# Performance work log

Measured on AMD Instinct MI355X. Metric: run time of the kernel, lower is better.

## Reference

```python
import jax, jax.numpy as jnp
import numpy as np

N_HEADS = 16
D_MODEL = 1024
D_KV = 64


def setup_inputs() -> dict:
    key = jax.random.key(0)
    ks = jax.random.split(key, 5)
    x = jax.random.normal(ks[0], (4, 2048, D_MODEL), dtype=jnp.float32)
    # per-head projections stacked: [H, D_MODEL, D_KV]
    WQ = jax.random.normal(ks[1], (N_HEADS, D_MODEL, D_KV), dtype=jnp.float32) * (D_MODEL ** -0.5)
    WK = jax.random.normal(ks[2], (N_HEADS, D_MODEL, D_KV), dtype=jnp.float32) * (D_MODEL ** -0.5)
    WV = jax.random.normal(ks[3], (N_HEADS, D_MODEL, D_KV), dtype=jnp.float32) * (D_MODEL ** -0.5)
    WO = jax.random.normal(ks[4], (N_HEADS * D_KV, D_MODEL), dtype=jnp.float32) * ((N_HEADS * D_KV) ** -0.5)
    return {"x": x, "WQ": WQ, "WK": WK, "WV": WV, "WO": WO}


def reference(x, WQ, WK, WV, WO):
    # Batched over heads instead of the original per-head Python loop.
    # q,k,v: [B, H, S, Dk]
    q = jnp.einsum('bsd,hdk->bhsk', x, WQ)
    k = jnp.einsum('bsd,hdk->bhsk', x, WK)
    v = jnp.einsum('bsd,hdk->bhsk', x, WV)
    scale = 1.0 / jnp.sqrt(jnp.asarray(q.shape[-1], q.dtype))
    scores = jnp.einsum('bhqk,bhsk->bhqs', q, k) * scale  # [B, H, S, S]
    attn = jax.nn.softmax(scores, axis=-1)
    o = jnp.einsum('bhqs,bhsk->bhqk', attn, v)            # [B, H, S, Dk]
    # concat heads along feature dim == transpose + reshape
    B, H, S, Dk = o.shape
    o = o.transpose(0, 2, 1, 3).reshape(B, S, H * Dk)
    return o @ WO
```

## Files before the change

### kernel.cpp

```cpp
#include <hip/hip_runtime.h>
#include <stdint.h>
#include <stddef.h>


typedef __attribute__((ext_vector_type(8))) short short8;
typedef __attribute__((ext_vector_type(4))) float floatx4;
typedef __attribute__((ext_vector_type(16))) float floatx16;

#define MFMA_BF16(a, b, c) __builtin_amdgcn_mfma_f32_16x16x32_bf16((a), (b), (c), 0, 0, 0)
#define MFMA32_BF16(a, b, c) __builtin_amdgcn_mfma_f32_32x32x16_bf16((a), (b), (c), 0, 0, 0)

__device__ __forceinline__ unsigned short f32_bf16(float f) {
  union { float f; unsigned u; } v; v.f = f;
  unsigned r = v.u + 0x7fffu + ((v.u >> 16) & 1u);
  return (unsigned short)(r >> 16);
}

__device__ __forceinline__ unsigned pack_bf16_rh(float a, float b) {
  unsigned ua = __float_as_uint(a) + 0x8000u;
  unsigned ub = __float_as_uint(b) + 0x8000u;
  return __builtin_amdgcn_perm(ub, ua, 0x07060302u);
}

__device__ __forceinline__ float fast_exp2(float x) {
#if __has_builtin(__builtin_amdgcn_exp2f)
  return __builtin_amdgcn_exp2f(x);
#else
  return exp2f(x);
#endif
}

__device__ __forceinline__ void g2l16(const void* g, void* l) {
  __builtin_amdgcn_global_load_lds((const __attribute__((address_space(1))) void*)g,
                                   (__attribute__((address_space(3))) void*)l,
                                   16, 0, 0);
}


__global__ __launch_bounds__(256) void cvt_x_k(const float* __restrict__ x,
                                               unsigned short* __restrict__ xb) {
  int i = (blockIdx.x * 256 + threadIdx.x) * 4;
  float4 v = *(const float4*)(x + i);
  ushort4 o;
  o.x = f32_bf16(v.x); o.y = f32_bf16(v.y); o.z = f32_bf16(v.z); o.w = f32_bf16(v.w);
  *(ushort4*)(xb + i) = o;
}

__global__ __launch_bounds__(256) void cvt_w_k(const float* __restrict__ WQ,
                                               const float* __restrict__ WK,
                                               const float* __restrict__ WV,
                                               const float* __restrict__ WO,
                                               unsigned short* __restrict__ Wqkv,
                                               unsigned short* __restrict__ WOt) {
  __shared__ unsigned short tile[64][72];
  const int bid = blockIdx.x;
  const int tid = threadIdx.x;
  if (bid < 768) {
    const int th = bid >> 4;
    const int typ = th >> 4, h = th & 15;
    const float* W = (typ == 0) ? WQ : ((typ == 1) ? WK : WV);
    const float* src = W + ((size_t)h * 1024 + (bid & 15) * 64) * 64;
    #pragma unroll
    for (int it = 0; it < 16; ++it) {
      int f = it * 256 + tid;
      int dk = f & 63, dl = f >> 6;
      tile[dk][dl] = f32_bf16(src[(size_t)dl * 64 + dk]);
    }
    __syncthreads();
    unsigned short* dst = Wqkv + (size_t)(typ * 1024 + h * 64) * 1024 + (bid & 15) * 64;
    #pragma unroll
    for (int it = 0; it < 16; ++it) {
      int f = it * 256 + tid;
      int d = f & 63, dk = f >> 6;
      dst[(size_t)dk * 1024 + d] = tile[dk][d];
    }
  } else {
    const int id2 = bid - 768;
    const int nt = (id2 & 15) * 64, kt = (id2 >> 4) * 64;
    #pragma unroll
    for (int it = 0; it < 16; ++it) {
      int f = it * 256 + tid;
      int n = f & 63, kl = f >> 6;
      tile[n][kl] = f32_bf16(WO[(size_t)(kt + kl) * 1024 + nt + n]);
    }
    __syncthreads();
    #pragma unroll
    for (int it = 0; it < 16; ++it) {
      int f = it * 256 + tid;
      int k = f & 63, nl = f >> 6;
      WOt[(size_t)(nt + nl) * 1024 + kt + k] = tile[nl][k];
    }
  }
}


__global__ __launch_bounds__(256, 2)
void gemm_qkv_k(const unsigned short* __restrict__ A,
                const unsigned short* __restrict__ Bt,
                unsigned short* __restrict__ Qo,
                unsigned short* __restrict__ Ko,
                unsigned short* __restrict__ Vo) {
  __shared__ __align__(16) unsigned short As[8192];
  __shared__ __align__(16) unsigned short Bs[8192];
  const int lane = threadIdx.x & 63;
  const int wave = threadIdx.x >> 6;
  const int quad = lane >> 4;
  const int t = lane & 15;
  const int wm = wave >> 1, wn = wave & 1;
  const int row0 = blockIdx.y * 128;
  const int col0 = blockIdx.x * 128;

  floatx4 acc[4][4];
  #pragma unroll
  for (int i = 0; i < 4; ++i)
    #pragma unroll
    for (int j = 0; j < 4; ++j) acc[i][j] = (floatx4)0.0f;

  for (int k0 = 0; k0 < 1024; k0 += 64) {
    #pragma unroll
    for (int i = 0; i < 4; ++i) {
      int s = (wave * 4 + i) * 64 + lane;
      int r = s >> 3, kc = (s & 7) ^ (r & 7);
      g2l16(A  + (size_t)(row0 + r) * 1024 + k0 + kc * 8, As + (wave * 4 + i) * 512);
      g2l16(Bt + (size_t)(col0 + r) * 1024 + k0 + kc * 8, Bs + (wave * 4 + i) * 512);
    }
    __syncthreads();
    #pragma unroll
    for (int kk = 0; kk < 2; ++kk) {
      short8 af[4], bf[4];
      #pragma unroll
      for (int mt = 0; mt < 4; ++mt) {
        int r = wm * 64 + mt * 16 + t;
        int kc = (kk * 4 + quad) ^ (r & 7);
        af[mt] = *(const short8*)(As + (r * 8 + kc) * 8);
      }
      #pragma unroll
      for (int nt = 0; nt < 4; ++nt) {
        int r = wn * 64 + nt * 16 + t;
        int kc = (kk * 4 + quad) ^ (r & 7);
        bf[nt] = *(const short8*)(Bs + (r * 8 + kc) * 8);
      }
      #pragma unroll
      for (int mt = 0; mt < 4; ++mt)
        #pragma unroll
        for (int nt = 0; nt < 4; ++nt)
          acc[mt][nt] = MFMA_BF16(af[mt], bf[nt], acc[mt][nt]);
    }
    __syncthreads();
  }

  const int typ = col0 >> 10;
  const float qscale = 0.18033688011112042f;
  const int qp = ((quad & 1) << 1) | (quad >> 1);
  #pragma unroll
  for (int mt = 0; mt < 4; ++mt) {
    int grow0 = row0 + wm * 64 + mt * 16 + quad * 4;
    int b = grow0 >> 11;
    int s = grow0 & 2047;
    #pragma unroll
    for (int nt = 0; nt < 4; ++nt) {
      int gcol = col0 + wn * 64 + nt * 16 + t;
      int rem = gcol & 1023;
      int h = rem >> 6, dk = rem & 63;
      int bhh = b * 16 + h;
      if (typ == 0) {
        #pragma unroll
        for (int rg = 0; rg < 4; ++rg)
          Qo[((size_t)bhh * 2048 + s + rg) * 64 + dk] = f32_bf16(acc[mt][nt][rg] * qscale);
      } else if (typ == 1) {
        #pragma unroll
        for (int rg = 0; rg < 4; ++rg)
          Ko[((size_t)bhh * 2048 + s + rg) * 64 + dk] = f32_bf16(acc[mt][nt][rg]);
      } else {
        ushort4 pv;
        pv.x = f32_bf16(acc[mt][nt][0]);
        pv.y = f32_bf16(acc[mt][nt][1]);
        pv.z = f32_bf16(acc[mt][nt][2]);
        pv.w = f32_bf16(acc[mt][nt][3]);
        int sp = (s & ~15) | (qp << 2);
        *(ushort4*)(Vo + ((size_t)bhh * 64 + dk) * 2048 + sp) = pv;
      }
    }
  }
}


__global__ __launch_bounds__(256, 2)
void attn_k(const unsigned short* __restrict__ Qg_,
            const unsigned short* __restrict__ Kg_,
            const unsigned short* __restrict__ Vg_,
            unsigned short* __restrict__ O) {
  __shared__ __align__(16) char smem[32768];
  const int lane = threadIdx.x & 63;
  const int wave = threadIdx.x >> 6;
  const int h32 = lane >> 5;
  const int c32 = lane & 31;
  const int bh = blockIdx.x;
  const int q0 = blockIdx.y * 256;
  const unsigned short* Qg = Qg_ + ((size_t)bh * 2048 + q0) * 64;
  const unsigned short* Kg = Kg_ + (size_t)bh * 2048 * 64;
  const unsigned short* Vg = Vg_ + (size_t)bh * 64 * 2048;

  short8 qf[2][4];
  #pragma unroll
  for (int g = 0; g < 2; ++g) {
    int rq = wave * 64 + g * 32 + c32;
    #pragma unroll
    for (int dc = 0; dc < 4; ++dc)
      qf[g][dc] = *(const short8*)(Qg + (size_t)rq * 64 + dc * 16 + h32 * 8);
  }

  union { unsigned u[4]; short8 s8; } onesf;
  #pragma unroll
  for (int i = 0; i < 4; ++i) onesf.u[i] = 0x3F803F80u;

  floatx16 acc[2][2], accs[2];
  #pragma unroll
  for (int g = 0; g < 2; ++g) {
    acc[g][0] = (floatx16)0.0f; acc[g][1] = (floatx16)0.0f; accs[g] = (floatx16)0.0f;
  }

  for (int s0 = 0; s0 < 2048; s0 += 128) {
    #pragma unroll
    for (int i = 0; i < 4; ++i) {
      int s = (wave * 4 + i) * 64 + lane;
      int rk = s >> 3, ck = (s & 7) ^ (rk & 7);
      g2l16(Kg + (size_t)(s0 + rk) * 64 + ck * 8, smem + s * 16);
      int rv = s >> 4, cv = (s & 15) ^ (rv & 7);
      g2l16(Vg + (size_t)rv * 2048 + s0 + cv * 8, smem + 16384 + s * 16);
    }
    __syncthreads();

    #pragma unroll
    for (int kb = 0; kb < 4; ++kb) {
      floatx16 sc0 = (floatx16)0.0f, sc1 = (floatx16)0.0f;
      #pragma unroll
      for (int dc = 0; dc < 4; ++dc) {
        int rk = kb * 32 + c32;
        int kc = (dc * 2 + h32) ^ (rk & 7);
        short8 kf = *(const short8*)(smem + (rk * 8 + kc) * 16);
        sc0 = MFMA32_BF16(kf, qf[0][dc], sc0);
        sc1 = MFMA32_BF16(kf, qf[1][dc], sc1);
      }
      unsigned pk0[8], pk1[8];
      #pragma unroll
      for (int i = 0; i < 8; ++i) {
        float a0 = fast_exp2(sc0[2 * i]), b0 = fast_exp2(sc0[2 * i + 1]);
        float a1 = fast_exp2(sc1[2 * i]), b1 = fast_exp2(sc1[2 * i + 1]);
        pk0[i] = pack_bf16_rh(a0, b0);
        pk1[i] = pack_bf16_rh(a1, b1);
      }
      #pragma unroll
      for (int st = 0; st < 2; ++st) {
        union { unsigned u[4]; short8 s8; } af0, af1;
        #pragma unroll
        for (int i = 0; i < 4; ++i) { af0.u[i] = pk0[4 * st + i]; af1.u[i] = pk1[4 * st + i]; }
        int cc = kb * 4 + st * 2 + h32;
        #pragma unroll
        for (int nb = 0; nb < 2; ++nb) {
          int rv = nb * 32 + c32;
          short8 bv = *(const short8*)(smem + 16384 + (rv * 16 + (cc ^ (rv & 7))) * 16);
          acc[0][nb] = MFMA32_BF16(af0.s8, bv, acc[0][nb]);
          acc[1][nb] = MFMA32_BF16(af1.s8, bv, acc[1][nb]);
        }
        accs[0] = MFMA32_BF16(af0.s8, onesf.s8, accs[0]);
        accs[1] = MFMA32_BF16(af1.s8, onesf.s8, accs[1]);
      }
    }
    __syncthreads();
  }

  const int b = bh >> 4, h = bh & 15;
  #pragma unroll
  for (int g = 0; g < 2; ++g) {
    #pragma unroll
    for (int gg = 0; gg < 4; ++gg) {
      #pragma unroll
      for (int rr = 0; rr < 4; ++rr) {
        int qrel = rr + 8 * gg + 4 * h32;
        float rl = 1.0f / accs[g][4 * gg + rr];
        int token = b * 2048 + q0 + wave * 64 + g * 32 + qrel;
        size_t base = (size_t)token * 1024 + h * 64;
        O[base + c32]      = f32_bf16(acc[g][0][4 * gg + rr] * rl);
        O[base + 32 + c32] = f32_bf16(acc[g][1][4 * gg + rr] * rl);
      }
    }
  }
}


__global__ __launch_bounds__(256, 2)
void gemm_out_k(const unsigned short* __restrict__ A,
                const unsigned short* __restrict__ Bt,
                float* __restrict__ C) {
  __shared__ __align__(16) unsigned short As[8192];
  __shared__ __align__(16) unsigned short Bs[8192];
  const int lane = threadIdx.x & 63;
  const int wave = threadIdx.x >> 6;
  const int quad = lane >> 4;
  const int t = lane & 15;
  const int wm = wave >> 1, wn = wave & 1;
  const int row0 = blockIdx.y * 128;
  const int col0 = blockIdx.x * 128;

  floatx4 acc[4][4];
  #pragma unroll
  for (int i = 0; i < 4; ++i)
    #pragma unroll
    for (int j = 0; j < 4; ++j) acc[i][j] = (floatx4)0.0f;

  for (int k0 = 0; k0 < 1024; k0 += 64) {
    #pragma unroll
    for (int i = 0; i < 4; ++i) {
      int s = (wave * 4 + i) * 64 + lane;
      int r = s >> 3, kc = (s & 7) ^ (r & 7);
      g2l16(A  + (size_t)(row0 + r) * 1024 + k0 + kc * 8, As + (wave * 4 + i) * 512);
      g2l16(Bt + (size_t)(col0 + r) * 1024 + k0 + kc * 8, Bs + (wave * 4 + i) * 512);
    }
    __syncthreads();
    #pragma unroll
    for (int kk = 0; kk < 2; ++kk) {
      short8 af[4], bf[4];
      #pragma unroll
      for (int mt = 0; mt < 4; ++mt) {
        int r = wm * 64 + mt * 16 + t;
        int kc = (kk * 4 + quad) ^ (r & 7);
        af[mt] = *(const short8*)(As + (r * 8 + kc) * 8);
      }
      #pragma unroll
      for (int nt = 0; nt < 4; ++nt) {
        int r = wn * 64 + nt * 16 + t;
        int kc = (kk * 4 + quad) ^ (r & 7);
        bf[nt] = *(const short8*)(Bs + (r * 8 + kc) * 8);
      }
      #pragma unroll
      for (int mt = 0; mt < 4; ++mt)
        #pragma unroll
        for (int nt = 0; nt < 4; ++nt)
          acc[mt][nt] = MFMA_BF16(af[mt], bf[nt], acc[mt][nt]);
    }
    __syncthreads();
  }

  #pragma unroll
  for (int mt = 0; mt < 4; ++mt) {
    int grow0 = row0 + wm * 64 + mt * 16 + quad * 4;
    #pragma unroll
    for (int nt = 0; nt < 4; ++nt) {
      int gcol = col0 + wn * 64 + nt * 16 + t;
      #pragma unroll
      for (int rg = 0; rg < 4; ++rg)
        C[(size_t)(grow0 + rg) * 1024 + gcol] = acc[mt][nt][rg];
    }
  }
}


extern "C" void kernel_launch(void* const* d_in, const int* in_sizes, int n_in,
                              void* d_out, int out_size, void* d_ws, size_t ws_size,
                              hipStream_t stream) {
  const float* x  = (const float*)d_in[0];
  const float* WQ = (const float*)d_in[1];
  const float* WK = (const float*)d_in[2];
  const float* WV = (const float*)d_in[3];
  const float* WO = (const float*)d_in[4];
  char* ws = (char*)d_ws;
  unsigned short* xb   = (unsigned short*)(ws);
  unsigned short* Wqkv = (unsigned short*)(ws + (size_t)16 * 1024 * 1024);
  unsigned short* WOt  = (unsigned short*)(ws + (size_t)22 * 1024 * 1024);
  unsigned short* Qb   = (unsigned short*)(ws + (size_t)24 * 1024 * 1024);
  unsigned short* Kb   = (unsigned short*)(ws + (size_t)40 * 1024 * 1024);
  unsigned short* Vb   = (unsigned short*)(ws + (size_t)56 * 1024 * 1024);
  float* out = (float*)d_out;

  cvt_x_k<<<8192, 256, 0, stream>>>(x, xb);
  cvt_w_k<<<1024, 256, 0, stream>>>(WQ, WK, WV, WO, Wqkv, WOt);
  gemm_qkv_k<<<dim3(24, 64), 256, 0, stream>>>(xb, Wqkv, Qb, Kb, Vb);
  attn_k<<<dim3(64, 8), 256, 0, stream>>>(Qb, Kb, Vb, xb );
  gemm_out_k<<<dim3(8, 64), 256, 0, stream>>>(xb, WOt, out);
}
```

Measured before the change: 262.6 us.

## Double-buffer K/V tiles in attention, use hardware bf16 pack and wave priorities

Splits the attention kernel's LDS into two 32KB buffers and prefetches the next K/V tile with async global-to-LDS loads while the current tile is computed. Waits use explicit vmcnt counts and raw barriers in place of __syncthreads. This is meant to hide global load latency behind the MFMA work. It also swaps the manual round-half bf16 packing for the v_cvt_pk_bf16_f32 instruction and raises wave priority around the MFMA sections. LDS use doubles to 64KB, which may limit the two-blocks-per-CU occupancy requested by the launch bounds.

Result: faster. 246.0 us (-6.3%).

```diff
diff --git a/kernel.cpp b/kernel.cpp
--- a/kernel.cpp
+++ b/kernel.cpp
@@ -16,10 +16,10 @@
   return (unsigned short)(r >> 16);
 }
 
-__device__ __forceinline__ unsigned pack_bf16_rh(float a, float b) {
-  unsigned ua = __float_as_uint(a) + 0x8000u;
-  unsigned ub = __float_as_uint(b) + 0x8000u;
-  return __builtin_amdgcn_perm(ub, ua, 0x07060302u);
+__device__ __forceinline__ unsigned cvt_pk_bf16(float a, float b) {
+  unsigned r;
+  asm("v_cvt_pk_bf16_f32 %0, %1, %2" : "=v"(r) : "v"(a), "v"(b));
+  return r;
 }
 
 __device__ __forceinline__ float fast_exp2(float x) {
@@ -190,7 +190,7 @@
             const unsigned short* __restrict__ Kg_,
             const unsigned short* __restrict__ Vg_,
             unsigned short* __restrict__ O) {
-  __shared__ __align__(16) char smem[32768];
+  __shared__ __align__(16) char smem[65536];
   const int lane = threadIdx.x & 63;
   const int wave = threadIdx.x >> 6;
   const int h32 = lane >> 5;
@@ -220,36 +220,53 @@
     acc[g][0] = (floatx16)0.0f; acc[g][1] = (floatx16)0.0f; accs[g] = (floatx16)0.0f;
   }
 
-  for (int s0 = 0; s0 < 2048; s0 += 128) {
+  auto stage = [&](int s0, int boff) {
     #pragma unroll
     for (int i = 0; i < 4; ++i) {
       int s = (wave * 4 + i) * 64 + lane;
       int rk = s >> 3, ck = (s & 7) ^ (rk & 7);
-      g2l16(Kg + (size_t)(s0 + rk) * 64 + ck * 8, smem + s * 16);
+      g2l16(Kg + (size_t)(s0 + rk) * 64 + ck * 8, smem + boff + s * 16);
       int rv = s >> 4, cv = (s & 15) ^ (rv & 7);
-      g2l16(Vg + (size_t)rv * 2048 + s0 + cv * 8, smem + 16384 + s * 16);
-    }
-    __syncthreads();
+      g2l16(Vg + (size_t)rv * 2048 + s0 + cv * 8, smem + boff + 16384 + s * 16);
+    }
+  };
+
+  stage(0, 0);
+  asm volatile("s_waitcnt vmcnt(0)\ns_barrier" ::: "memory");
+
+  for (int it = 0; it < 16; ++it) {
+    const int boff = (it & 1) << 15;
+    if (it < 15) {
+      stage((it + 1) * 128, boff ^ 32768);
+      asm volatile("s_waitcnt vmcnt(8)\ns_barrier" ::: "memory");
+    } else {
+      asm volatile("s_waitcnt vmcnt(0)\ns_barrier" ::: "memory");
+    }
+    const char* kbase = smem + boff;
+    const char* vbase = smem + boff + 16384;
 
     #pragma unroll
     for (int kb = 0; kb < 4; ++kb) {
       floatx16 sc0 = (floatx16)0.0f, sc1 = (floatx16)0.0f;
+      __builtin_amdgcn_s_setprio(1);
       #pragma unroll
       for (int dc = 0; dc < 4; ++dc) {
         int rk = kb * 32 + c32;
         int kc = (dc * 2 + h32) ^ (rk & 7);
-        short8 kf = *(const short8*)(smem + (rk * 8 + kc) * 16);
+        short8 kf = *(const short8*)(kbase + (rk * 8 + kc) * 16);
         sc0 = MFMA32_BF16(kf, qf[0][dc], sc0);
         sc1 = MFMA32_BF16(kf, qf[1][dc], sc1);
       }
+      __builtin_amdgcn_s_setprio(0);
       unsigned pk0[8], pk1[8];
       #pragma unroll
       for (int i = 0; i < 8; ++i) {
         float a0 = fast_exp2(sc0[2 * i]), b0 = fast_exp2(sc0[2 * i + 1]);
         float a1 = fast_exp2(sc1[2 * i]), b1 = fast_exp2(sc1[2 * i + 1]);
-        pk0[i] = pack_bf16_rh(a0, b0);
-        pk1[i] = pack_bf16_rh(a1, b1);
-      }
+        pk0[i] = cvt_pk_bf16(a0, b0);
+        pk1[i] = cvt_pk_bf16(a1, b1);
+      }
+      __builtin_amdgcn_s_setprio(1);
       #pragma unroll
       for (int st = 0; st < 2; ++st) {
         union { unsigned u[4]; short8 s8; } af0, af1;
@@ -259,15 +276,16 @@
         #pragma unroll
         for (int nb = 0; nb < 2; ++nb) {
           int rv = nb * 32 + c32;
-          short8 bv = *(const short8*)(smem + 16384 + (rv * 16 + (cc ^ (rv & 7))) * 16);
+          short8 bv = *(const short8*)(vbase + (rv * 16 + (cc ^ (rv & 7))) * 16);
           acc[0][nb] = MFMA32_BF16(af0.s8, bv, acc[0][nb]);
           acc[1][nb] = MFMA32_BF16(af1.s8, bv, acc[1][nb]);
         }
         accs[0] = MFMA32_BF16(af0.s8, onesf.s8, accs[0]);
         accs[1] = MFMA32_BF16(af1.s8, onesf.s8, accs[1]);
       }
-    }
-    __syncthreads();
+      __builtin_amdgcn_s_setprio(0);
+    }
+    asm volatile("s_barrier" ::: "memory");
   }
 
   const int b = bh >> 4, h = bh & 15;
```

## Halve attention query tile per wave, raise occupancy, add setprio and hardware bf16 pack

Applied to the files above, without the earlier changes.

Each wave in the attention kernel now handles 32 query rows instead of 64, so the grid doubles to 1024 blocks and launch bounds request 4 blocks per CU. This cuts register pressure and improves latency hiding, but each K/V tile loaded into LDS now serves half as many queries, doubling K/V load traffic. The kernel also wraps the MFMA sections in s_setprio and replaces the manual round-half-up bf16 pack with the v_cvt_pk_bf16_f32 instruction.

New measurement: 255.4 us. 2.7% less time.

```diff
diff --git a/kernel.cpp b/kernel.cpp
--- a/kernel.cpp
+++ b/kernel.cpp
@@ -16,10 +16,10 @@
   return (unsigned short)(r >> 16);
 }
 
-__device__ __forceinline__ unsigned pack_bf16_rh(float a, float b) {
-  unsigned ua = __float_as_uint(a) + 0x8000u;
-  unsigned ub = __float_as_uint(b) + 0x8000u;
-  return __builtin_amdgcn_perm(ub, ua, 0x07060302u);
+__device__ __forceinline__ unsigned cvt_pk_bf16(float a, float b) {
+  unsigned r;
+  asm("v_cvt_pk_bf16_f32 %0, %1, %2" : "=v"(r) : "v"(a), "v"(b));
+  return r;
 }
 
 __device__ __forceinline__ float fast_exp2(float x) {
@@ -185,7 +185,7 @@
 }
 
 
-__global__ __launch_bounds__(256, 2)
+__global__ __launch_bounds__(256, 4)
 void attn_k(const unsigned short* __restrict__ Qg_,
             const unsigned short* __restrict__ Kg_,
             const unsigned short* __restrict__ Vg_,
@@ -196,29 +196,25 @@
   const int h32 = lane >> 5;
   const int c32 = lane & 31;
   const int bh = blockIdx.x;
-  const int q0 = blockIdx.y * 256;
+  const int q0 = blockIdx.y * 128;
   const unsigned short* Qg = Qg_ + ((size_t)bh * 2048 + q0) * 64;
   const unsigned short* Kg = Kg_ + (size_t)bh * 2048 * 64;
   const unsigned short* Vg = Vg_ + (size_t)bh * 64 * 2048;
 
-  short8 qf[2][4];
-  #pragma unroll
-  for (int g = 0; g < 2; ++g) {
-    int rq = wave * 64 + g * 32 + c32;
+  short8 qf[4];
+  {
+    int rq = wave * 32 + c32;
     #pragma unroll
     for (int dc = 0; dc < 4; ++dc)
-      qf[g][dc] = *(const short8*)(Qg + (size_t)rq * 64 + dc * 16 + h32 * 8);
+      qf[dc] = *(const short8*)(Qg + (size_t)rq * 64 + dc * 16 + h32 * 8);
   }
 
   union { unsigned u[4]; short8 s8; } onesf;
   #pragma unroll
   for (int i = 0; i < 4; ++i) onesf.u[i] = 0x3F803F80u;
 
-  floatx16 acc[2][2], accs[2];
-  #pragma unroll
-  for (int g = 0; g < 2; ++g) {
-    acc[g][0] = (floatx16)0.0f; acc[g][1] = (floatx16)0.0f; accs[g] = (floatx16)0.0f;
-  }
+  floatx16 acc[2], accs;
+  acc[0] = (floatx16)0.0f; acc[1] = (floatx16)0.0f; accs = (floatx16)0.0f;
 
   for (int s0 = 0; s0 < 2048; s0 += 128) {
     #pragma unroll
@@ -233,57 +229,53 @@
 
     #pragma unroll
     for (int kb = 0; kb < 4; ++kb) {
-      floatx16 sc0 = (floatx16)0.0f, sc1 = (floatx16)0.0f;
+      floatx16 sc = (floatx16)0.0f;
+      __builtin_amdgcn_s_setprio(1);
       #pragma unroll
       for (int dc = 0; dc < 4; ++dc) {
         int rk = kb * 32 + c32;
         int kc = (dc * 2 + h32) ^ (rk & 7);
         short8 kf = *(const short8*)(smem + (rk * 8 + kc) * 16);
-        sc0 = MFMA32_BF16(kf, qf[0][dc], sc0);
-        sc1 = MFMA32_BF16(kf, qf[1][dc], sc1);
-      }
-      unsigned pk0[8], pk1[8];
+        sc = MFMA32_BF16(kf, qf[dc], sc);
+      }
+      __builtin_amdgcn_s_setprio(0);
+      unsigned pk[8];
       #pragma unroll
       for (int i = 0; i < 8; ++i) {
-        float a0 = fast_exp2(sc0[2 * i]), b0 = fast_exp2(sc0[2 * i + 1]);
-        float a1 = fast_exp2(sc1[2 * i]), b1 = fast_exp2(sc1[2 * i + 1]);
-        pk0[i] = pack_bf16_rh(a0, b0);
-        pk1[i] = pack_bf16_rh(a1, b1);
-      }
+        float a = fast_exp2(sc[2 * i]), b = fast_exp2(sc[2 * i + 1]);
+        pk[i] = cvt_pk_bf16(a, b);
+      }
+      __builtin_amdgcn_s_setprio(1);
       #pragma unroll
       for (int st = 0; st < 2; ++st) {
-        union { unsigned u[4]; short8 s8; } af0, af1;
-        #pragma unroll
-        for (int i = 0; i < 4; ++i) { af0.u[i] = pk0[4 * st + i]; af1.u[i] = pk1[4 * st + i]; }
+        union { unsigned u[4]; short8 s8; } af;
+        #pragma unroll
+        for (int i = 0; i < 4; ++i) af.u[i] = pk[4 * st + i];
         int cc = kb * 4 + st * 2 + h32;
         #pragma unroll
         for (int nb = 0; nb < 2; ++nb) {
           int rv = nb * 32 + c32;
           short8 bv = *(const short8*)(smem + 16384 + (rv * 16 + (cc ^ (rv & 7))) * 16);
-          acc[0][nb] = MFMA32_BF16(af0.s8, bv, acc[0][nb]);
-          acc[1][nb] = MFMA32_BF16(af1.s8, bv, acc[1][nb]);
+          acc[nb] = MFMA32_BF16(af.s8, bv, acc[nb]);
         }
-        accs[0] = MFMA32_BF16(af0.s8, onesf.s8, accs[0]);
-        accs[1] = MFMA32_BF16(af1.s8, onesf.s8, accs[1]);
-      }
+        accs = MFMA32_BF16(af.s8, onesf.s8, accs);
+      }
+      __builtin_amdgcn_s_setprio(0);
     }
     __syncthreads();
   }
 
   const int b = bh >> 4, h = bh & 15;
   #pragma unroll
-  for (int g = 0; g < 2; ++g) {
-    #pragma unroll
-    for (int gg = 0; gg < 4; ++gg) {
-      #pragma unroll
-      for (int rr = 0; rr < 4; ++rr) {
-        int qrel = rr + 8 * gg + 4 * h32;
-        float rl = 1.0f / accs[g][4 * gg + rr];
-        int token = b * 2048 + q0 + wave * 64 + g * 32 + qrel;
-        size_t base = (size_t)token * 1024 + h * 64;
-        O[base + c32]      = f32_bf16(acc[g][0][4 * gg + rr] * rl);
-        O[base + 32 + c32] = f32_bf16(acc[g][1][4 * gg + rr] * rl);
-      }
+  for (int gg = 0; gg < 4; ++gg) {
+    #pragma unroll
+    for (int rr = 0; rr < 4; ++rr) {
+      int qrel = rr + 8 * gg + 4 * h32;
+      float rl = 1.0f / accs[4 * gg + rr];
+      int token = b * 2048 + q0 + wave * 32 + qrel;
+      size_t base = (size_t)token * 1024 + h * 64;
+      O[base + c32]      = f32_bf16(acc[0][4 * gg + rr] * rl);
+      O[base + 32 + c32] = f32_bf16(acc[1][4 * gg + rr] * rl);
     }
   }
 }
@@ -376,6 +368,6 @@
   cvt_x_k<<<8192, 256, 0, stream>>>(x, xb);
   cvt_w_k<<<1024, 256, 0, stream>>>(WQ, WK, WV, WO, Wqkv, WOt);
   gemm_qkv_k<<<dim3(24, 64), 256, 0, stream>>>(xb, Wqkv, Qb, Kb, Vb);
-  attn_k<<<dim3(64, 8), 256, 0, stream>>>(Qb, Kb, Vb, xb );
+  attn_k<<<dim3(64, 16), 256, 0, stream>>>(Qb, Kb, Vb, xb );
   gemm_out_k<<<dim3(8, 64), 256, 0, stream>>>(xb, WOt, out);
 }
```
